# Optimization experiments

Measured on AMD Instinct MI355X. Metric: run time of the kernel, lower is better.

Reference implementation:

```python
import jax, jax.numpy as jnp
import numpy as np

NUM_HEADS = 8
NUM_GROUPS = 32
EPS = 1e-5


def group_norm(x, scale, bias):
    # x: (b, c, t)
    b, c, t = x.shape
    xg = x.reshape(b, NUM_GROUPS, c // NUM_GROUPS, t)
    mean = xg.mean(axis=(2, 3), keepdims=True)
    var = xg.var(axis=(2, 3), keepdims=True)
    xn = ((xg - mean) * jax.lax.rsqrt(var + EPS)).reshape(b, c, t)
    return xn * scale[None, :, None] + bias[None, :, None]


def setup_inputs() -> dict:
    key = jax.random.key(0)
    ks = jax.random.split(key, 3)
    b, c, h, w = 16, 512, 32, 32
    x = jax.random.normal(ks[0], (b, c, h, w), dtype=jnp.float32)
    gn_scale = jnp.ones((c,), jnp.float32)
    gn_bias = jnp.zeros((c,), jnp.float32)
    w_qkv = jax.random.normal(ks[1], (3 * c, c), jnp.float32) * (c ** -0.5)
    b_qkv = jnp.zeros((3 * c,), jnp.float32)
    w_proj = jax.random.normal(ks[2], (c, c), jnp.float32) * (c ** -0.5)
    b_proj = jnp.zeros((c,), jnp.float32)
    return {"x": x, "gn_scale": gn_scale, "gn_bias": gn_bias,
            "w_qkv": w_qkv, "b_qkv": b_qkv, "w_proj": w_proj, "b_proj": b_proj}


def reference(x, gn_scale, gn_bias, w_qkv, b_qkv, w_proj, b_proj):
    b, c, h, w = x.shape
    t = h * w
    xf = x.reshape(b, c, t)
    xn = group_norm(xf, gn_scale, gn_bias)
    # 1x1 conv1d == channel matmul: (b, 3c, t)
    qkv = jnp.einsum('oc,bct->bot', w_qkv, xn) + b_qkv[None, :, None]
    dh = c // NUM_HEADS
    qkv = qkv.reshape(b * NUM_HEADS, 3 * dh, t)
    q, k, v = jnp.split(qkv, 3, axis=1)  # each (b*H, dh, t)
    scale = dh ** -0.25
    logits = jnp.einsum('bct,bcs->bts', q * scale, k * scale)
    weight = jax.nn.softmax(logits.astype(jnp.float32), axis=-1).astype(logits.dtype)
    attn = jnp.einsum('bts,bcs->bct', weight, v)  # (b*H, dh, t)
    attn = attn.reshape(b, c, t)
    out = jnp.einsum('oc,bct->bot', w_proj, attn) + b_proj[None, :, None]
    return (xf + out).reshape(b, c, h, w)
```

## Files before the change

### kernel.cpp

```cpp
#include <hip/hip_runtime.h>
#include <hip/hip_bf16.h>

typedef __hip_bfloat16 bf16;
typedef __attribute__((ext_vector_type(8))) short short8;
typedef __attribute__((ext_vector_type(4))) short short4v;
typedef __attribute__((ext_vector_type(4))) float float4v;
typedef __attribute__((ext_vector_type(16))) float f32x16;
typedef __attribute__((ext_vector_type(4))) int int4v;

__device__ __forceinline__ float b2f(bf16 v) { return __bfloat162float(v); }
__device__ __forceinline__ bf16  f2b(float v) { return __float2bfloat16(v); }
__device__ __forceinline__ short f2s(float v) { bf16 h = f2b(v); return *reinterpret_cast<short*>(&h); }
__device__ __forceinline__ float s2f(short s) { bf16 h; *reinterpret_cast<short*>(&h) = s; return b2f(h); }
__device__ __forceinline__ short8 ld8(const bf16* p) { return *(const short8*)p; }

__device__ __forceinline__ float ldin(const void* p, size_t i, int f32) {
  return f32 ? ((const float*)p)[i] : b2f(((const bf16*)p)[i]);
}

__device__ __forceinline__ float4v mfma16(short8 a, short8 b, float4v c) {
  return __builtin_amdgcn_mfma_f32_16x16x32_bf16(a, b, c, 0, 0, 0);
}
__device__ __forceinline__ f32x16 mfma32(short8 a, short8 b, f32x16 c) {
  return __builtin_amdgcn_mfma_f32_32x32x16_bf16(a, b, c, 0, 0, 0);
}
__device__ __forceinline__ int cvtpk(float a, float b) {
  int r; asm("v_cvt_pk_bf16_f32 %0, %1, %2" : "=v"(r) : "v"(a), "v"(b)); return r;
}
__device__ __forceinline__ void plswap(int& x, int& y) {
  asm("v_permlane32_swap_b32 %0, %1" : "+v"(x), "+v"(y));
}

__device__ __forceinline__ void gload16(const void* g, void* l) {
  __builtin_amdgcn_global_load_lds((__attribute__((address_space(1))) void*)(void*)g,
                                   (__attribute__((address_space(3))) void*)l, 16, 0, 0);
}

__device__ __forceinline__ int self_detect(const void* x, int* sh) {
  const int tid = threadIdx.x;
  if (tid == 0) *sh = 0;
  __syncthreads();
  int local = 0;
  const short8* xv = (const short8*)x;
#pragma unroll
  for (int i = 0; i < 4; i++) {
    const short8 v = xv[tid + i * 256];
#pragma unroll
    for (int j = 0; j < 8; j++)
      if ((((unsigned short)v[j]) & 0x7F80u) == 0x7F80u) local = 1;
  }
  if (local) atomicOr(sh, 1);
  __syncthreads();
  return *sh;
}

#define K2SCALE 0.18033688011112042f
#define TSTRIDE 72

__global__ __launch_bounds__(256) void pre_kernel(const void* __restrict__ s1, bf16* __restrict__ d1,
                                                  const void* __restrict__ s2, bf16* __restrict__ d2,
                                                  const void* __restrict__ s3, bf16* __restrict__ d3,
                                                  const void* __restrict__ s4, bf16* __restrict__ d4,
                                                  const void* __restrict__ x,
                                                  float2* __restrict__ stats) {
  const int blk = blockIdx.x;
  const int tid = threadIdx.x;
  __shared__ int fl;
  __shared__ float rs[4], rss[4];
  const int f32 = self_detect(x, &fl);

  if (blk < 1027) {
    const void* src; bf16* dst; int base, n;
    if (blk < 768)       { src = s1; dst = d1; base = blk;        n = 786432; }
    else if (blk < 1024) { src = s2; dst = d2; base = blk - 768;  n = 262144; }
    else if (blk < 1026) { src = s3; dst = d3; base = blk - 1024; n = 1536;   }
    else                 { src = s4; dst = d4; base = 0;          n = 512;    }
    const int i0 = (base * 256 + tid) * 4;
    if (i0 + 3 < n) {
      short4v pk;
      if (f32) {
        const float4v v = *(const float4v*)((const float*)src + i0);
#pragma unroll
        for (int j = 0; j < 4; j++) pk[j] = f2s(v[j]);
      } else {
        pk = *(const short4v*)((const bf16*)src + i0);
      }
      *(short4v*)(dst + i0) = pk;
    } else {
      for (int j = 0; j < 4; j++) {
        int i = i0 + j;
        if (i < n) dst[i] = f2b(ldin(src, i, f32));
      }
    }
    return;
  }

  const int bg = blk - 1027;
  const int GSZ = 16 * 1024;
  const size_t base = (size_t)bg * GSZ;

  float s = 0.f, ss = 0.f;
  if (f32) {
    const float4v* xp = (const float4v*)((const float*)x + base) + tid;
#pragma unroll
    for (int i = 0; i < 16; i++) {
      float4v v = xp[i * 256];
#pragma unroll
      for (int j = 0; j < 4; j++) { s += v[j]; ss += v[j] * v[j]; }
    }
  } else {
    const short8* xp = (const short8*)((const bf16*)x + base) + tid;
#pragma unroll
    for (int i = 0; i < 8; i++) {
      short8 v = xp[i * 256];
#pragma unroll
      for (int j = 0; j < 8; j++) { float f = s2f(v[j]); s += f; ss += f * f; }
    }
  }
  for (int off = 32; off > 0; off >>= 1) {
    s  += __shfl_down(s, off);
    ss += __shfl_down(ss, off);
  }
  const int wave = tid >> 6, lane = tid & 63;
  if (lane == 0) { rs[wave] = s; rss[wave] = ss; }
  __syncthreads();
  if (tid == 0) {
    s  = rs[0] + rs[1] + rs[2] + rs[3];
    ss = rss[0] + rss[1] + rss[2] + rss[3];
    const float mean = s * (1.f / GSZ);
    const float var  = ss * (1.f / GSZ) - mean * mean;
    stats[bg] = make_float2(mean, rsqrtf(var + 1e-5f));
  }
}

__global__ __launch_bounds__(256) void gn_apply_kernel(const void* __restrict__ x,
                                                       const void* __restrict__ gsc,
                                                       const void* __restrict__ gbi,
                                                       const float2* __restrict__ stats,
                                                       bf16* __restrict__ xn) {
  const int b = blockIdx.y;
  const int t0 = blockIdx.x * 32;
  const int cs = blockIdx.z * 128;
  const int tid = threadIdx.x;

  __shared__ int fl;
  __shared__ float Aa[128], Bb[128];
  __shared__ short T[32][136];
  const int f32 = self_detect(x, &fl);

  if (tid < 128) {
    const int c = cs + tid;
    const float2 st = stats[b * 32 + (c >> 4)];
    const float sc = ldin(gsc, c, f32), bi = ldin(gbi, c, f32);
    Aa[tid] = st.y * sc;
    Bb[tid] = bi - st.x * st.y * sc;
  }
  __syncthreads();

  const int row = tid >> 3;
  const int t4 = (tid & 7) * 4;
  if (f32) {
    const float* xb = (const float*)x + ((size_t)(b * 512 + cs)) * 1024 + t0 + t4;
#pragma unroll
    for (int st = 0; st < 4; st++) {
      const int c = row + st * 32;
      const float4v v = *(const float4v*)(xb + (size_t)c * 1024);
      const float aa = Aa[c], bb = Bb[c];
#pragma unroll
      for (int j = 0; j < 4; j++) T[t4 + j][c] = f2s(v[j] * aa + bb);
    }
  } else {
    const bf16* xb = (const bf16*)x + ((size_t)(b * 512 + cs)) * 1024 + t0 + t4;
#pragma unroll
    for (int st = 0; st < 4; st++) {
      const int c = row + st * 32;
      const short4v v = *(const short4v*)(xb + (size_t)c * 1024);
      const float aa = Aa[c], bb = Bb[c];
#pragma unroll
      for (int j = 0; j < 4; j++) T[t4 + j][c] = f2s(s2f(v[j]) * aa + bb);
    }
  }
  __syncthreads();

#pragma unroll
  for (int j = 0; j < 2; j++) {
    const int ci = tid + j * 256;
    const int t2 = ci >> 4;
    const int c8 = (ci & 15) * 8;
    const short8 v = *(const short8*)&T[t2][c8];
    *(short8*)&xn[((size_t)(b * 1024 + t0 + t2)) * 512 + cs + c8] = v;
  }
}

__global__ __launch_bounds__(256) void qkv_kernel(const bf16* __restrict__ Wb,
                                                  const bf16* __restrict__ biasb,
                                                  const bf16* __restrict__ xn,
                                                  bf16* __restrict__ Qt,
                                                  bf16* __restrict__ Kt,
                                                  bf16* __restrict__ Vb) {
  const int bat = blockIdx.z;
  const int M0 = blockIdx.y * 128;
  const int N0 = blockIdx.x * 128;
  __shared__ short smem[18432];

  const int tid = threadIdx.x;
  const int w = tid >> 6, lane = tid & 63;
  const int col = lane & 15, g = lane >> 4;
  const int wm = (w & 1) * 64, wn = (w >> 1) * 64;

  float4v acc[4][4];
#pragma unroll
  for (int i = 0; i < 4; i++)
#pragma unroll
    for (int j = 0; j < 4; j++) acc[i][j] = (float4v)(0.f);

  int srco[2], dstb[2];
#pragma unroll
  for (int i = 0; i < 2; i++) {
    const int Gb = i * 256 + w * 64;
    dstb[i] = Gb * 8;
    const int G = Gb + lane;
    srco[i] = (G >> 2) * 512 + (G & 3) * 8;
  }
  const bf16* Ab  = Wb + (size_t)M0 * 512;
  const bf16* Bb2 = xn + ((size_t)bat * 1024 + N0) * 512;

#pragma unroll
  for (int i = 0; i < 2; i++) {
    gload16(Ab + srco[i],  &smem[dstb[i]]);
    gload16(Bb2 + srco[i], &smem[4096 + dstb[i]]);
  }
  __syncthreads();

  for (int it = 0; it < 16; ++it) {
    const int pb = it & 1;
    if (it < 15) {
      const int kn = it * 32 + 32;
      const int nb = (1 - pb) * 8192;
#pragma unroll
      for (int i = 0; i < 2; i++) {
        gload16(Ab + kn + srco[i],  &smem[nb + dstb[i]]);
        gload16(Bb2 + kn + srco[i], &smem[nb + 4096 + dstb[i]]);
      }
    }
    const short* Ap = &smem[pb * 8192];
    const short* Bp = Ap + 4096;
    short8 af[4], bf4[4];
#pragma unroll
    for (int mt = 0; mt < 4; mt++) af[mt] = *(const short8*)&Ap[(wm + mt * 16 + col) * 32 + g * 8];
#pragma unroll
    for (int nt = 0; nt < 4; nt++) bf4[nt] = *(const short8*)&Bp[(wn + nt * 16 + col) * 32 + g * 8];
#pragma unroll
    for (int mt = 0; mt < 4; mt++)
#pragma unroll
      for (int nt = 0; nt < 4; nt++) acc[mt][nt] = mfma16(af[mt], bf4[nt], acc[mt][nt]);
    __syncthreads();
  }

  const int sec = (M0 + wm) >> 6;
  const int h = sec / 3, kind = sec % 3;
  const size_t bh = (size_t)bat * 8 + h;
  const float qs = (kind == 0) ? K2SCALE : 1.f;
  short* Tw = smem + w * 4608;

  float bv[4][4];
#pragma unroll
  for (int mt = 0; mt < 4; mt++)
#pragma unroll
    for (int r = 0; r < 4; r++) bv[mt][r] = b2f(biasb[M0 + wm + mt * 16 + g * 4 + r]);

  if (kind == 2) {
#pragma unroll
    for (int mt = 0; mt < 4; mt++)
#pragma unroll
      for (int nt = 0; nt < 4; nt++)
#pragma unroll
        for (int r = 0; r < 4; r++) {
          const int lo = mt * 16 + g * 4 + r;
          const int lt = nt * 16 + col;
          Tw[lo * TSTRIDE + lt] = f2s(acc[mt][nt][r] + bv[mt][r]);
        }
#pragma unroll
    for (int j = 0; j < 8; j++) {
      const int lo = j * 8 + (lane >> 3);
      const int gr = lane & 7;
      short8 v = *(const short8*)&Tw[lo * TSTRIDE + gr * 8];
      *(short8*)(Vb + (bh * 64 + lo) * 1024 + N0 + wn + gr * 8) = v;
    }
  } else {
#pragma unroll
    for (int mt = 0; mt < 4; mt++)
#pragma unroll
      for (int nt = 0; nt < 4; nt++) {
        short4v pk;
#pragma unroll
        for (int r = 0; r < 4; r++) pk[r] = f2s((acc[mt][nt][r] + bv[mt][r]) * qs);
        *(short4v*)&Tw[(nt * 16 + col) * TSTRIDE + mt * 16 + g * 4] = pk;
      }
    bf16* dst = (kind == 0) ? Qt : Kt;
#pragma unroll
    for (int j = 0; j < 8; j++) {
      const int tl = j * 8 + (lane >> 3), c8 = (lane & 7) * 8;
      short8 v = *(const short8*)&Tw[tl * TSTRIDE + c8];
      *(short8*)(dst + (bh * 1024 + N0 + wn + tl) * 64 + c8) = v;
    }
  }
}

__global__ __launch_bounds__(256, 2) void attn_kernel(const bf16* __restrict__ Qt,
                                                      const bf16* __restrict__ Kt,
                                                      const bf16* __restrict__ Vb,
                                                      bf16* __restrict__ xattn) {
  const int bh = blockIdx.x;
  const int t0 = blockIdx.y * 256;
  const int b = bh >> 3, h = bh & 7;
  const int tid = threadIdx.x;
  const int w = tid >> 6, lane = tid & 63;
  const int qv = lane & 31, hh = lane >> 5;
  const int q0 = t0 + w * 64;

  __shared__ short Ks[8192];
  __shared__ short Vs[8192];

  const bf16* kbase = Kt + (size_t)bh * 65536;
  const bf16* vbase = Vb + (size_t)bh * 65536;

  int ksrc[2], vsrc[2];
  const int ldst0 = w * 1024, ldst1 = w * 1024 + 512;
#pragma unroll
  for (int i = 0; i < 2; i++) {
    const int G = w * 128 + i * 64 + lane;
    const int a = G >> 8, ks = (G >> 6) & 3, qvs = (G >> 1) & 31, hhs = G & 1;
    const int co = (ks * 2 + hhs) * 8;
    ksrc[i] = (a * 32 + qvs) * 64 + co;
    vsrc[i] = (a * 32 + qvs) * 1024 + co;
  }
  const int rb = (qv * 2 + hh) * 8;

  short8 qb[2][4];
#pragma unroll
  for (int qt = 0; qt < 2; qt++)
#pragma unroll
    for (int ks = 0; ks < 4; ks++)
      qb[qt][ks] = ld8(Qt + ((size_t)bh * 1024 + q0 + qt * 32 + qv) * 64 + ks * 16 + hh * 8);

  f32x16 O[2][2];
#pragma unroll
  for (int qt = 0; qt < 2; qt++)
#pragma unroll
    for (int o = 0; o < 2; o++) O[qt][o] = (f32x16)(0.f);
  float l[2] = {0.f, 0.f};
  short8 pa[2][4];
  const f32x16 FZ = (f32x16)(0.f);

  gload16(kbase + ksrc[0], &Ks[ldst0]);
  gload16(kbase + ksrc[1], &Ks[ldst1]);
  gload16(vbase + vsrc[0], &Vs[ldst0]);
  gload16(vbase + vsrc[1], &Vs[ldst1]);
  __syncthreads();

#define SMAX(S, qt, a)                                                          \
  {                                                                             \
    _Pragma("unroll")                                                           \
    for (int j = 0; j < 16; j++) S[j] = __builtin_amdgcn_exp2f(S[j]);           \
    l[qt] += (((S[0] + S[1]) + (S[2] + S[3])) + ((S[4] + S[5]) + (S[6] + S[7])))\
       + (((S[8] + S[9]) + (S[10] + S[11])) + ((S[12] + S[13]) + (S[14] + S[15]))); \
    _Pragma("unroll")                                                           \
    for (int kp = 0; kp < 2; kp++) {                                            \
      int X  = cvtpk(S[8 * kp + 0], S[8 * kp + 1]);                             \
      int Y  = cvtpk(S[8 * kp + 4], S[8 * kp + 5]);                             \
      int X2 = cvtpk(S[8 * kp + 2], S[8 * kp + 3]);                             \
      int Y2 = cvtpk(S[8 * kp + 6], S[8 * kp + 7]);                             \
      plswap(X, Y);                                                             \
      plswap(X2, Y2);                                                           \
      const int4v wv = {X, X2, Y, Y2};                                          \
      pa[qt][(a) * 2 + kp] = __builtin_bit_cast(short8, wv);                    \
    }                                                                           \
  }

#pragma unroll 2
  for (int it = 0; it < 16; ++it) {
    const int cur = (it & 1) * 4096;
    const int nxt = 4096 - cur;
    if (it < 15) {
      gload16(kbase + (it + 1) * 4096 + ksrc[0], &Ks[nxt + ldst0]);
      gload16(kbase + (it + 1) * 4096 + ksrc[1], &Ks[nxt + ldst1]);
      gload16(vbase + (it + 1) * 64 + vsrc[0],   &Vs[nxt + ldst0]);
      gload16(vbase + (it + 1) * 64 + vsrc[1],   &Vs[nxt + ldst1]);
    }
#pragma unroll
    for (int a = 0; a < 2; a++) {
      short8 kf[4];
#pragma unroll
      for (int ks = 0; ks < 4; ks++)
        kf[ks] = *(const short8*)&Ks[cur + (a * 4 + ks) * 512 + rb];
#pragma unroll
      for (int qt = 0; qt < 2; qt++) {
        f32x16 S = mfma32(kf[0], qb[qt][0], FZ);
#pragma unroll
        for (int ks = 1; ks < 4; ks++) S = mfma32(kf[ks], qb[qt][ks], S);
        SMAX(S, qt, a);
      }
    }
#pragma unroll
    for (int o = 0; o < 2; o++) {
      short8 vf[4];
#pragma unroll
      for (int ks = 0; ks < 4; ks++)
        vf[ks] = *(const short8*)&Vs[cur + (o * 4 + ks) * 512 + rb];
#pragma unroll
      for (int qt = 0; qt < 2; qt++)
#pragma unroll
        for (int ks = 0; ks < 4; ks++)
          O[qt][o] = mfma32(pa[qt][ks], vf[ks], O[qt][o]);
    }
    __syncthreads();
  }
#undef SMAX

#pragma unroll
  for (int qt = 0; qt < 2; qt++) {
    float lt = l[qt] + __shfl_xor(l[qt], 32);
    const float inv = 1.f / lt;
    float* lf = (float*)Ks + w * 64 + qt * 32;
    lf[qv] = inv;

    bf16* ob = xattn + ((size_t)b * 1024 + q0 + qt * 32 + 4 * hh) * 512 + h * 64 + qv;
#pragma unroll
    for (int r = 0; r < 16; r++) {
      const int qoff = (r & 3) + 8 * (r >> 2);
      const float iv = lf[qoff + 4 * hh];
      ob[(size_t)qoff * 512]      = f2b(O[qt][0][r] * iv);
      ob[(size_t)qoff * 512 + 32] = f2b(O[qt][1][r] * iv);
    }
  }
}

__global__ __launch_bounds__(256) void proj_kernel(const bf16* __restrict__ Wp,
                                                   const bf16* __restrict__ biasb,
                                                   const bf16* __restrict__ xattn,
                                                   const void* __restrict__ res,
                                                   void* __restrict__ out) {
  const int bat = blockIdx.z;
  const int M0 = blockIdx.y * 128;
  const int N0 = blockIdx.x * 128;
  __shared__ short smem[18432];
  __shared__ int fl;
  const int f32 = self_detect(res, &fl);

  const int tid = threadIdx.x;
  const int w = tid >> 6, lane = tid & 63;
  const int col = lane & 15, g = lane >> 4;
  const int wm = (w & 1) * 64, wn = (w >> 1) * 64;

  float4v acc[4][4];
#pragma unroll
  for (int i = 0; i < 4; i++)
#pragma unroll
    for (int j = 0; j < 4; j++) acc[i][j] = (float4v)(0.f);

  int srco[2], dstb[2];
#pragma unroll
  for (int i = 0; i < 2; i++) {
    const int Gb = i * 256 + w * 64;
    dstb[i] = Gb * 8;
    const int G = Gb + lane;
    srco[i] = (G >> 2) * 512 + (G & 3) * 8;
  }
  const bf16* Ab  = Wp + (size_t)M0 * 512;
  const bf16* Bb2 = xattn + ((size_t)bat * 1024 + N0) * 512;

#pragma unroll
  for (int i = 0; i < 2; i++) {
    gload16(Ab + srco[i],  &smem[dstb[i]]);
    gload16(Bb2 + srco[i], &smem[4096 + dstb[i]]);
  }
  __syncthreads();

  for (int it = 0; it < 16; ++it) {
    const int pb = it & 1;
    if (it < 15) {
      const int kn = it * 32 + 32;
      const int nb = (1 - pb) * 8192;
#pragma unroll
      for (int i = 0; i < 2; i++) {
        gload16(Ab + kn + srco[i],  &smem[nb + dstb[i]]);
        gload16(Bb2 + kn + srco[i], &smem[nb + 4096 + dstb[i]]);
      }
    }
    const short* Ap = &smem[pb * 8192];
    const short* Bp = Ap + 4096;
    short8 af[4], bf4[4];
#pragma unroll
    for (int mt = 0; mt < 4; mt++) af[mt] = *(const short8*)&Ap[(wm + mt * 16 + col) * 32 + g * 8];
#pragma unroll
    for (int nt = 0; nt < 4; nt++) bf4[nt] = *(const short8*)&Bp[(wn + nt * 16 + col) * 32 + g * 8];
#pragma unroll
    for (int mt = 0; mt < 4; mt++)
#pragma unroll
      for (int nt = 0; nt < 4; nt++) acc[mt][nt] = mfma16(af[mt], bf4[nt], acc[mt][nt]);
    __syncthreads();
  }

  short* Tw = smem + w * 4608;
  float bv[4][4];
#pragma unroll
  for (int mt = 0; mt < 4; mt++)
#pragma unroll
    for (int r = 0; r < 4; r++) bv[mt][r] = b2f(biasb[M0 + wm + mt * 16 + g * 4 + r]);

#pragma unroll
  for (int mt = 0; mt < 4; mt++)
#pragma unroll
    for (int nt = 0; nt < 4; nt++)
#pragma unroll
      for (int r = 0; r < 4; r++) {
        const int lo = mt * 16 + g * 4 + r;
        const int lt = nt * 16 + col;
        Tw[lo * TSTRIDE + lt] = f2s(acc[mt][nt][r] + bv[mt][r]);
      }
#pragma unroll
  for (int j = 0; j < 8; j++) {
    const int lo = j * 8 + (lane >> 3);
    const int gr = lane & 7;
    short8 v = *(const short8*)&Tw[lo * TSTRIDE + gr * 8];
    const int o = M0 + wm + lo;
    const size_t ci = ((size_t)bat * 512 + o) * 1024 + N0 + wn + gr * 8;
    if (f32) {
      const float4v r0 = *(const float4v*)((const float*)res + ci);
      const float4v r1 = *(const float4v*)((const float*)res + ci + 4);
      float4v o0, o1;
#pragma unroll
      for (int e = 0; e < 4; e++) o0[e] = s2f(v[e]) + r0[e];
#pragma unroll
      for (int e = 0; e < 4; e++) o1[e] = s2f(v[e + 4]) + r1[e];
      *(float4v*)((float*)out + ci) = o0;
      *(float4v*)((float*)out + ci + 4) = o1;
    } else {
      const short8 rv = *(const short8*)((const bf16*)res + ci);
      short8 ov;
#pragma unroll
      for (int e = 0; e < 8; e++)
        ov[e] = f2s(s2f(v[e]) + s2f(rv[e]));
      *(short8*)((bf16*)out + ci) = ov;
    }
  }
}

extern "C" void kernel_launch(void* const* d_in, const int* in_sizes, int n_in,
                              void* d_out, int out_size, void* d_ws, size_t ws_size,
                              hipStream_t stream) {
  const void* x      = d_in[0];
  const void* gsc    = d_in[1];
  const void* gbi    = d_in[2];
  const void* w_qkv  = d_in[3];
  const void* b_qkv  = d_in[4];
  const void* w_proj = d_in[5];
  const void* b_proj = d_in[6];

  char* p = (char*)d_ws;
  float2* stats = (float2*)p;              p += 1024 * sizeof(float2);
  bf16*   xn    = (bf16*)p;                p += (size_t)16 * 1024 * 512 * 2;
  bf16*   Qt    = (bf16*)p;                p += (size_t)128 * 1024 * 64 * 2;
  bf16*   Kt    = (bf16*)p;                p += (size_t)128 * 1024 * 64 * 2;
  bf16*   Vb    = (bf16*)p;                p += (size_t)128 * 64 * 1024 * 2;
  bf16*   Wqb   = (bf16*)p;                p += (size_t)1536 * 512 * 2;
  bf16*   Wpb   = (bf16*)p;                p += (size_t)512 * 512 * 2;
  bf16*   Bqb   = (bf16*)p;                p += (size_t)1536 * 2;
  bf16*   Bpb   = (bf16*)p;                p += (size_t)512 * 2;
  bf16*   xattn = (bf16*)p;

  pre_kernel<<<1539, 256, 0, stream>>>(w_qkv, Wqb, w_proj, Wpb,
                                       b_qkv, Bqb, b_proj, Bpb,
                                       x, stats);
  gn_apply_kernel<<<dim3(32, 16, 4), 256, 0, stream>>>(x, gsc, gbi, stats, xn);
  qkv_kernel<<<dim3(8, 12, 16), 256, 0, stream>>>(Wqb, Bqb, xn, Qt, Kt, Vb);
  attn_kernel<<<dim3(128, 4), 256, 0, stream>>>(Qt, Kt, Vb, xattn);
  proj_kernel<<<dim3(8, 4, 16), 256, 0, stream>>>(Wpb, Bpb, xattn, x, d_out);
}
```

Before: 194.2 us.

## Fuse group-norm statistics and apply into one register-resident kernel

Moves the group-norm mean/variance reduction out of the weight-conversion kernel into a new 1024-thread kernel. Each block loads 32 channels of one batch into registers once, reduces statistics for two groups, normalizes, and writes the transposed bf16 output through shared memory. This removes the second global read of x and the stats round-trip through workspace. In exchange it launches only 256 large blocks and adds eight barrier-separated transpose rounds, and the shared-memory transpose reads are strided.

```diff
diff --git a/kernel.cpp b/kernel.cpp
--- a/kernel.cpp
+++ b/kernel.cpp
@@ -42,9 +42,8 @@
   __syncthreads();
   int local = 0;
   const short8* xv = (const short8*)x;
-#pragma unroll
-  for (int i = 0; i < 4; i++) {
-    const short8 v = xv[tid + i * 256];
+  for (int idx = tid; idx < 1024; idx += blockDim.x) {
+    const short8 v = xv[idx];
 #pragma unroll
     for (int j = 0; j < 8; j++)
       if ((((unsigned short)v[j]) & 0x7F80u) == 0x7F80u) local = 1;
@@ -61,134 +60,108 @@
                                                   const void* __restrict__ s2, bf16* __restrict__ d2,
                                                   const void* __restrict__ s3, bf16* __restrict__ d3,
                                                   const void* __restrict__ s4, bf16* __restrict__ d4,
-                                                  const void* __restrict__ x,
-                                                  float2* __restrict__ stats) {
+                                                  const void* __restrict__ x) {
   const int blk = blockIdx.x;
   const int tid = threadIdx.x;
   __shared__ int fl;
-  __shared__ float rs[4], rss[4];
   const int f32 = self_detect(x, &fl);
 
-  if (blk < 1027) {
-    const void* src; bf16* dst; int base, n;
-    if (blk < 768)       { src = s1; dst = d1; base = blk;        n = 786432; }
-    else if (blk < 1024) { src = s2; dst = d2; base = blk - 768;  n = 262144; }
-    else if (blk < 1026) { src = s3; dst = d3; base = blk - 1024; n = 1536;   }
-    else                 { src = s4; dst = d4; base = 0;          n = 512;    }
-    const int i0 = (base * 256 + tid) * 4;
-    if (i0 + 3 < n) {
-      short4v pk;
-      if (f32) {
-        const float4v v = *(const float4v*)((const float*)src + i0);
-#pragma unroll
-        for (int j = 0; j < 4; j++) pk[j] = f2s(v[j]);
-      } else {
-        pk = *(const short4v*)((const bf16*)src + i0);
-      }
-      *(short4v*)(dst + i0) = pk;
+  const void* src; bf16* dst; int base, n;
+  if (blk < 768)       { src = s1; dst = d1; base = blk;        n = 786432; }
+  else if (blk < 1024) { src = s2; dst = d2; base = blk - 768;  n = 262144; }
+  else if (blk < 1026) { src = s3; dst = d3; base = blk - 1024; n = 1536;   }
+  else                 { src = s4; dst = d4; base = 0;          n = 512;    }
+  const int i0 = (base * 256 + tid) * 4;
+  if (i0 + 3 < n) {
+    short4v pk;
+    if (f32) {
+      const float4v v = *(const float4v*)((const float*)src + i0);
+#pragma unroll
+      for (int j = 0; j < 4; j++) pk[j] = f2s(v[j]);
     } else {
-      for (int j = 0; j < 4; j++) {
-        int i = i0 + j;
-        if (i < n) dst[i] = f2b(ldin(src, i, f32));
-      }
-    }
-    return;
-  }
-
-  const int bg = blk - 1027;
-  const int GSZ = 16 * 1024;
-  const size_t base = (size_t)bg * GSZ;
+      pk = *(const short4v*)((const bf16*)src + i0);
+    }
+    *(short4v*)(dst + i0) = pk;
+  } else {
+    for (int j = 0; j < 4; j++) {
+      int i = i0 + j;
+      if (i < n) dst[i] = f2b(ldin(src, i, f32));
+    }
+  }
+}
+
+__global__ __launch_bounds__(1024) void gn_fused_kernel(const void* __restrict__ x,
+                                                        const void* __restrict__ gsc,
+                                                        const void* __restrict__ gbi,
+                                                        bf16* __restrict__ xn) {
+  const int c0 = blockIdx.x * 32;
+  const int b  = blockIdx.y;
+  const int tid = threadIdx.x;
+  const int r = tid >> 5;
+  const int q = tid & 31;
+
+  __shared__ int fl;
+  __shared__ float ws[16], wss[16], stM[2], stI[2];
+  __shared__ short T[32 * 132];
+  const int f32 = self_detect(x, &fl);
+
+  float4v vv[8];
+  const size_t rowbase = ((size_t)(b * 512 + c0 + r)) * 1024 + q * 4;
+  if (f32) {
+    const float* xr = (const float*)x + rowbase;
+#pragma unroll
+    for (int j = 0; j < 8; j++) vv[j] = *(const float4v*)(xr + j * 128);
+  } else {
+    const bf16* xr = (const bf16*)x + rowbase;
+#pragma unroll
+    for (int j = 0; j < 8; j++) {
+      const short4v s4 = *(const short4v*)(xr + j * 128);
+#pragma unroll
+      for (int k = 0; k < 4; k++) vv[j][k] = s2f(s4[k]);
+    }
+  }
 
   float s = 0.f, ss = 0.f;
-  if (f32) {
-    const float4v* xp = (const float4v*)((const float*)x + base) + tid;
-#pragma unroll
-    for (int i = 0; i < 16; i++) {
-      float4v v = xp[i * 256];
-#pragma unroll
-      for (int j = 0; j < 4; j++) { s += v[j]; ss += v[j] * v[j]; }
-    }
-  } else {
-    const short8* xp = (const short8*)((const bf16*)x + base) + tid;
-#pragma unroll
-    for (int i = 0; i < 8; i++) {
-      short8 v = xp[i * 256];
-#pragma unroll
-      for (int j = 0; j < 8; j++) { float f = s2f(v[j]); s += f; ss += f * f; }
-    }
-  }
+#pragma unroll
+  for (int j = 0; j < 8; j++)
+#pragma unroll
+    for (int k = 0; k < 4; k++) { const float f = vv[j][k]; s += f; ss += f * f; }
   for (int off = 32; off > 0; off >>= 1) {
     s  += __shfl_down(s, off);
     ss += __shfl_down(ss, off);
   }
-  const int wave = tid >> 6, lane = tid & 63;
-  if (lane == 0) { rs[wave] = s; rss[wave] = ss; }
-  __syncthreads();
-  if (tid == 0) {
-    s  = rs[0] + rs[1] + rs[2] + rs[3];
-    ss = rss[0] + rss[1] + rss[2] + rss[3];
-    const float mean = s * (1.f / GSZ);
-    const float var  = ss * (1.f / GSZ) - mean * mean;
-    stats[bg] = make_float2(mean, rsqrtf(var + 1e-5f));
-  }
-}
-
-__global__ __launch_bounds__(256) void gn_apply_kernel(const void* __restrict__ x,
-                                                       const void* __restrict__ gsc,
-                                                       const void* __restrict__ gbi,
-                                                       const float2* __restrict__ stats,
-                                                       bf16* __restrict__ xn) {
-  const int b = blockIdx.y;
-  const int t0 = blockIdx.x * 32;
-  const int cs = blockIdx.z * 128;
-  const int tid = threadIdx.x;
-
-  __shared__ int fl;
-  __shared__ float Aa[128], Bb[128];
-  __shared__ short T[32][136];
-  const int f32 = self_detect(x, &fl);
-
-  if (tid < 128) {
-    const int c = cs + tid;
-    const float2 st = stats[b * 32 + (c >> 4)];
-    const float sc = ldin(gsc, c, f32), bi = ldin(gbi, c, f32);
-    Aa[tid] = st.y * sc;
-    Bb[tid] = bi - st.x * st.y * sc;
-  }
-  __syncthreads();
-
-  const int row = tid >> 3;
-  const int t4 = (tid & 7) * 4;
-  if (f32) {
-    const float* xb = (const float*)x + ((size_t)(b * 512 + cs)) * 1024 + t0 + t4;
-#pragma unroll
-    for (int st = 0; st < 4; st++) {
-      const int c = row + st * 32;
-      const float4v v = *(const float4v*)(xb + (size_t)c * 1024);
-      const float aa = Aa[c], bb = Bb[c];
-#pragma unroll
-      for (int j = 0; j < 4; j++) T[t4 + j][c] = f2s(v[j] * aa + bb);
-    }
-  } else {
-    const bf16* xb = (const bf16*)x + ((size_t)(b * 512 + cs)) * 1024 + t0 + t4;
-#pragma unroll
-    for (int st = 0; st < 4; st++) {
-      const int c = row + st * 32;
-      const short4v v = *(const short4v*)(xb + (size_t)c * 1024);
-      const float aa = Aa[c], bb = Bb[c];
-#pragma unroll
-      for (int j = 0; j < 4; j++) T[t4 + j][c] = f2s(s2f(v[j]) * aa + bb);
-    }
-  }
-  __syncthreads();
-
-#pragma unroll
-  for (int j = 0; j < 2; j++) {
-    const int ci = tid + j * 256;
-    const int t2 = ci >> 4;
-    const int c8 = (ci & 15) * 8;
-    const short8 v = *(const short8*)&T[t2][c8];
-    *(short8*)&xn[((size_t)(b * 1024 + t0 + t2)) * 512 + cs + c8] = v;
+  const int wv = tid >> 6, lane = tid & 63;
+  if (lane == 0) { ws[wv] = s; wss[wv] = ss; }
+  __syncthreads();
+  if (tid < 2) {
+    float S = 0.f, SS = 0.f;
+#pragma unroll
+    for (int i = 0; i < 8; i++) { S += ws[tid * 8 + i]; SS += wss[tid * 8 + i]; }
+    const float mean = S * (1.f / 16384.f);
+    const float var  = SS * (1.f / 16384.f) - mean * mean;
+    stM[tid] = mean;
+    stI[tid] = rsqrtf(var + 1e-5f);
+  }
+  __syncthreads();
+
+  const int gi = r >> 4;
+  const float sc = ldin(gsc, c0 + r, f32), bi = ldin(gbi, c0 + r, f32);
+  const float aa = stI[gi] * sc;
+  const float bb = bi - stM[gi] * stI[gi] * sc;
+
+  const int to = tid >> 3, c4 = (tid & 7) * 4;
+#pragma unroll
+  for (int j = 0; j < 8; j++) {
+    short4v pk;
+#pragma unroll
+    for (int k = 0; k < 4; k++) pk[k] = f2s(vv[j][k] * aa + bb);
+    *(short4v*)&T[r * 132 + q * 4] = pk;
+    __syncthreads();
+    short4v ov;
+#pragma unroll
+    for (int k = 0; k < 4; k++) ov[k] = T[(c4 + k) * 132 + to];
+    *(short4v*)&xn[((size_t)(b * 1024 + j * 128 + to)) * 512 + c0 + c4] = ov;
+    __syncthreads();
   }
 }
 
@@ -559,7 +532,6 @@
   const void* b_proj = d_in[6];
 
   char* p = (char*)d_ws;
-  float2* stats = (float2*)p;              p += 1024 * sizeof(float2);
   bf16*   xn    = (bf16*)p;                p += (size_t)16 * 1024 * 512 * 2;
   bf16*   Qt    = (bf16*)p;                p += (size_t)128 * 1024 * 64 * 2;
   bf16*   Kt    = (bf16*)p;                p += (size_t)128 * 1024 * 64 * 2;
@@ -570,10 +542,9 @@
   bf16*   Bpb   = (bf16*)p;                p += (size_t)512 * 2;
   bf16*   xattn = (bf16*)p;
 
-  pre_kernel<<<1539, 256, 0, stream>>>(w_qkv, Wqb, w_proj, Wpb,
-                                       b_qkv, Bqb, b_proj, Bpb,
-                                       x, stats);
-  gn_apply_kernel<<<dim3(32, 16, 4), 256, 0, stream>>>(x, gsc, gbi, stats, xn);
+  pre_kernel<<<1027, 256, 0, stream>>>(w_qkv, Wqb, w_proj, Wpb,
+                                       b_qkv, Bqb, b_proj, Bpb, x);
+  gn_fused_kernel<<<dim3(16, 16), 1024, 0, stream>>>(x, gsc, gbi, xn);
   qkv_kernel<<<dim3(8, 12, 16), 256, 0, stream>>>(Wqb, Bqb, xn, Qt, Kt, Vb);
   attn_kernel<<<dim3(128, 4), 256, 0, stream>>>(Qt, Kt, Vb, xattn);
   proj_kernel<<<dim3(8, 4, 16), 256, 0, stream>>>(Wpb, Bpb, xattn, x, d_out);
```

New measurement: 191.3 us. No clear change (-1.5%).
